# Kernel optimization log

Hardware: AMD Instinct MI355X
Metric: run time of the kernel (lower is better)

The kernel has to match this reference:

```python
import jax, jax.numpy as jnp
import numpy as np

MAX_DEPTH = 8          # inner-node depths 1..8; leaves at depth 9
LMBDA = 0.1            # args.lmbda; per-node lmbda = LMBDA * 2**(-depth)
EPS = 1e-6


def setup_inputs() -> dict:
    key = jax.random.key(0)
    ks = jax.random.split(key, 7)
    B, D, O = 16384, 2048, 1000
    n_inner = 2 ** MAX_DEPTH - 1   # 255
    n_leaf = 2 ** MAX_DEPTH       # 256
    x = jax.random.normal(ks[0], (B, D), dtype=jnp.float32)
    target = jax.random.randint(ks[1], (B,), 0, O)
    y = jax.nn.one_hot(target, O, dtype=jnp.float32)  # target_onehot
    W = jax.random.normal(ks[2], (n_inner, D), dtype=jnp.float32) / np.sqrt(D)
    b = jax.random.normal(ks[3], (n_inner,), dtype=jnp.float32) * 0.01
    beta = jax.random.normal(ks[4], (n_inner,), dtype=jnp.float32)
    leaf_params = jax.random.normal(ks[5], (n_leaf, O), dtype=jnp.float32)
    return {"x": x, "y": y, "W": W, "b": b, "beta": beta, "leaf_params": leaf_params}


def reference(x, y, W, b, beta, leaf_params):
    """Faithful vectorized version of SoftDecisionTree.cal_loss.
    Inner nodes are stored in level-order (heap) layout, left-to-right
    within each level, matching the left-first recursion of cal_prob.
    Returns (loss, output) like cal_loss.
    """
    B = x.shape[0]
    dt = x.dtype
    # All inner-node gates in one fused GEMM: sigmoid(beta * (x @ w + b))
    probs = jax.nn.sigmoid(beta * (x @ W.T + b))  # [B, n_inner]

    path = jnp.ones((B, 1), dt)  # path_prob_init
    C = jnp.asarray(0.0, dt)
    idx = 0
    for d in range(1, MAX_DEPTH + 1):  # small fixed loop over tree levels
        n = 2 ** (d - 1)
        p = probs[:, idx:idx + n]      # gate probs for this level's nodes [B, n]
        if d < MAX_DEPTH:              # get_penalty skips nodes whose children are leaves
            denom = jnp.sum(path, axis=0)                  # [n]
            denom = jnp.where(denom == 0, EPS, denom)
            alpha = jnp.sum(p * path, axis=0) / denom      # [n]
            alpha = jnp.clip(alpha, EPS, 1.0 - EPS)
            lmbda = LMBDA * 2.0 ** (-d)
            C = C - jnp.sum(lmbda * 0.5 * (jnp.log(alpha) + jnp.log1p(-alpha)))
        # children: left gets path*(1-p), right gets path*p, interleaved
        path = jnp.stack([path * (1.0 - p), path * p], axis=-1).reshape(B, 2 * n)
        idx += n
    # path: [B, n_leaf] leaf arrival probabilities (left-to-right leaf order)

    logQ = jax.nn.log_softmax(leaf_params, axis=-1)  # [n_leaf, O]
    TQ = y @ logQ.T                                  # [B, n_leaf]: y . log Q per leaf
    loss_term = jnp.mean(jnp.sum(path * TQ, axis=1))
    loss = -loss_term + C

    best = jnp.argmax(path, axis=1)   # first max, matches the '<' update order
    output = jnp.exp(logQ)[best]      # [B, O] max_Q
    return loss, output
```

## Files before the change

kernel.cpp:

```cpp
#include <hip/hip_runtime.h>


typedef __attribute__((ext_vector_type(8))) short short8;
typedef __attribute__((ext_vector_type(4))) float f32x4;

#define DIM 2048
#define NCLS 1000
#define NINNER 255
#define NPAD 256
#define BM 32
#define CHUNKF 128
#define NCHUNK 16

__device__ __forceinline__ unsigned cvt2bf(float a, float b) {
  return ((__float_as_uint(a) + 0x8000u) >> 16) | ((__float_as_uint(b) + 0x8000u) & 0xFFFF0000u);
}

__device__ __forceinline__ void async_copy16(const float* gsrc, void* ldst) {
  __builtin_amdgcn_global_load_lds(
      (const __attribute__((address_space(1))) unsigned int*)(gsrc),
      (__attribute__((address_space(3))) unsigned int*)(ldst), 16, 0, 0);
}

__global__ __launch_bounds__(256) void prep_w(const float* __restrict__ W,
                                              const float* __restrict__ b,
                                              const float* __restrict__ beta,
                                              unsigned short* __restrict__ WbP,
                                              float* __restrict__ bp,
                                              float* __restrict__ betap) {
  int f = blockIdx.x * 256 + threadIdx.x;
  int kt = f >> 10;
  int T = (f >> 6) & 15;
  int l = f & 63;
  int row = T * 16 + (l & 15);
  int k0 = kt * 32 + (l >> 4) * 8;
  uint4 o = make_uint4(0u, 0u, 0u, 0u);
  if (row < NINNER) {
    const float* src = W + (size_t)row * DIM + k0;
    o.x = cvt2bf(src[0], src[1]);
    o.y = cvt2bf(src[2], src[3]);
    o.z = cvt2bf(src[4], src[5]);
    o.w = cvt2bf(src[6], src[7]);
  }
  *(uint4*)(WbP + (size_t)f * 8) = o;
  if (f < NPAD) {
    bp[f] = (f < NINNER) ? b[f] : 0.f;
    betap[f] = (f < NINNER) ? beta[f] : 0.f;
  }
}

__global__ __launch_bounds__(256) void leaf_softmax(const float* __restrict__ leaf,
                                                    float* __restrict__ logQT,
                                                    float* __restrict__ Q) {
  int l = blockIdx.x, t = threadIdx.x;
  const float* row = leaf + (size_t)l * NCLS;
  __shared__ float red[256];
  float mx = -3.4e38f;
  for (int j = t; j < NCLS; j += 256) mx = fmaxf(mx, row[j]);
  red[t] = mx; __syncthreads();
  for (int s = 128; s; s >>= 1) { if (t < s) red[t] = fmaxf(red[t], red[t + s]); __syncthreads(); }
  mx = red[0]; __syncthreads();
  float sm = 0.f;
  for (int j = t; j < NCLS; j += 256) sm += __expf(row[j] - mx);
  red[t] = sm; __syncthreads();
  for (int s = 128; s; s >>= 1) { if (t < s) red[t] += red[t + s]; __syncthreads(); }
  float lse = mx + __logf(red[0]);
  for (int j = t; j < NCLS; j += 256) {
    float lg = row[j] - lse;
    logQT[(size_t)j * NPAD + l] = lg;
    Q[(size_t)l * NCLS + j] = __expf(lg);
  }
}

__global__ __launch_bounds__(256) void find_targets(const float* __restrict__ y,
                                                    int* __restrict__ tgt) {
  int wv = threadIdx.x >> 6, lane = threadIdx.x & 63;
  int r = blockIdx.x * 4 + wv;
  const float4* yr = (const float4*)(y + (size_t)r * NCLS);
  int found = 0x7fffffff;
#pragma unroll
  for (int i = 0; i < 4; ++i) {
    int j4 = i * 64 + lane;
    if (j4 < 250) {
      float4 v = yr[j4];
      if (v.x > 0.5f) found = min(found, 4 * j4 + 0);
      if (v.y > 0.5f) found = min(found, 4 * j4 + 1);
      if (v.z > 0.5f) found = min(found, 4 * j4 + 2);
      if (v.w > 0.5f) found = min(found, 4 * j4 + 3);
    }
  }
  for (int off = 32; off; off >>= 1) found = min(found, __shfl_down(found, off));
  if (lane == 0) tgt[r] = found;
}

__device__ __forceinline__ void chunk_mma(f32x4 (&ac)[2][4], const float* Ab,
                                          const unsigned short* bptr, int c,
                                          int frow, int fq) {
#pragma unroll
  for (int s = 0; s < 4; ++s) {
    int kt = c * 4 + s;
    short8 bfr[4];
#pragma unroll
    for (int nt = 0; nt < 4; ++nt)
      bfr[nt] = *(const short8*)(bptr + ((size_t)kt * 1024 + nt * 64) * 8);
    short8 afr[2];
#pragma unroll
    for (int mt = 0; mt < 2; ++mt) {
      int R = mt * 16 + frow;
      int r7 = R & 7;
      const float4* base = (const float4*)(Ab + R * 128 + s * 32);
      float4 va = base[(2 * fq) ^ r7];
      float4 vb = base[(2 * fq + 1) ^ r7];
      union { uint4 u; short8 s8; } cv;
      cv.u.x = cvt2bf(va.x, va.y);
      cv.u.y = cvt2bf(va.z, va.w);
      cv.u.z = cvt2bf(vb.x, vb.y);
      cv.u.w = cvt2bf(vb.z, vb.w);
      afr[mt] = cv.s8;
    }
#pragma unroll
    for (int nt = 0; nt < 4; ++nt)
#pragma unroll
      for (int mt = 0; mt < 2; ++mt)
        ac[mt][nt] = __builtin_amdgcn_mfma_f32_16x16x32_bf16(afr[mt], bfr[nt], ac[mt][nt], 0, 0, 0);
  }
}

__global__ __launch_bounds__(256, 2) void gemm_tree(
    const float* __restrict__ x, const unsigned short* __restrict__ WbP,
    const float* __restrict__ bp, const float* __restrict__ betap,
    const float* __restrict__ logQT, const int* __restrict__ tgt,
    float* __restrict__ acc, int* __restrict__ best) {
  __shared__ __align__(16) float As[2][4096];
  __shared__ float s0s[127], s1s[127], sdot;

  int tid = threadIdx.x;
  int lane = tid & 63, wave = tid >> 6;
  int frow = lane & 15, fq = lane >> 4;
  int m_base = blockIdx.x * BM;

  if (tid < 127) { s0s[tid] = 0.f; s1s[tid] = 0.f; }
  if (tid == 255) sdot = 0.f;

  const float* asrc[4];
  int aoff[4];
#pragma unroll
  for (int a = 0; a < 4; ++a) {
    int L = a * 4096 + tid * 16;
    int r = L >> 9;
    int j = (L >> 4) & 31;
    int c16 = (j & 24) | ((j & 7) ^ (r & 7));
    asrc[a] = x + (size_t)(m_base + r) * DIM + c16 * 4;
    aoff[a] = L;
  }

  const unsigned short* bptr = WbP + ((size_t)wave * 256 + lane) * 8;

  f32x4 accA[2][4] = {}, accB[2][4] = {};

#pragma unroll
  for (int a = 0; a < 4; ++a) async_copy16(asrc[a], (char*)As[0] + aoff[a]);
  __syncthreads();

  for (int c = 0; c < NCHUNK; ++c) {
    if (c + 1 < NCHUNK) {
      float* nb = As[(c + 1) & 1];
#pragma unroll
      for (int a = 0; a < 4; ++a)
        async_copy16(asrc[a] + (c + 1) * CHUNKF, (char*)nb + aoff[a]);
    }
    const float* Ab = As[c & 1];
    if (c < 8) chunk_mma(accA, Ab, bptr, c, frow, fq);
    else       chunk_mma(accB, Ab, bptr, c, frow, fq);
    __syncthreads();
  }

  float* Ps = &As[0][0];
#pragma unroll
  for (int mt = 0; mt < 2; ++mt)
#pragma unroll
    for (int nt = 0; nt < 4; ++nt)
#pragma unroll
      for (int rg = 0; rg < 4; ++rg)
        Ps[(mt * 16 + fq * 4 + rg) * 256 + wave * 64 + nt * 16 + frow] =
            accA[mt][nt][rg] + accB[mt][nt][rg];
  __syncthreads();

  {
    float bc = bp[tid], bec = betap[tid];
#pragma unroll 4
    for (int i = 0; i < 32; ++i) {
      float v = Ps[i * 256 + tid];
      Ps[i * 256 + tid] = 1.f / (1.f + __expf(-bec * (v + bc)));
    }
  }
  __syncthreads();

  float wdot = 0.f;
  float s0r[7] = {}, s1r[7] = {};
  for (int it = 0; it < 8; ++it) {
    int rl = wave * 8 + it;
    int r = m_base + rl;
    const float* wsp = Ps + rl * 256;
    int tg = tgt[r];
    float pp = 1.f;
#pragma unroll
    for (int d = 1; d <= 6; ++d) {
      int idx = (1 << (d - 1)) - 1 + (lane >> (7 - d));
      float p = wsp[idx];
      s0r[d - 1] += pp;
      s1r[d - 1] += p * pp;
      pp *= ((lane >> (6 - d)) & 1) ? p : (1.f - p);
    }
    float p7 = wsp[63 + lane];
    s0r[6] += pp;
    s1r[6] += p7 * pp;
    float pL = pp * (1.f - p7), pR = pp * p7;
    float p8a = wsp[127 + 2 * lane], p8b = wsp[128 + 2 * lane];
    float lf0 = pL * (1.f - p8a), lf1 = pL * p8a;
    float lf2 = pR * (1.f - p8b), lf3 = pR * p8b;
    float4 lq = *(const float4*)(logQT + (size_t)tg * NPAD + lane * 4);
    wdot += lf0 * lq.x + lf1 * lq.y + lf2 * lq.z + lf3 * lq.w;
    float bv = lf0; int bi = 4 * lane;
    if (lf1 > bv) { bv = lf1; bi = 4 * lane + 1; }
    if (lf2 > bv) { bv = lf2; bi = 4 * lane + 2; }
    if (lf3 > bv) { bv = lf3; bi = 4 * lane + 3; }
    for (int off = 32; off; off >>= 1) {
      float ov = __shfl_down(bv, off);
      int oi = __shfl_down(bi, off);
      if (ov > bv || (ov == bv && oi < bi)) { bv = ov; bi = oi; }
    }
    if (lane == 0) best[r] = bi;
  }
#pragma unroll
  for (int d = 1; d <= 6; ++d) {
    int idx = (1 << (d - 1)) - 1 + (lane >> (7 - d));
    if ((lane & ((1 << (7 - d)) - 1)) == 0) {
      atomicAdd(&s0s[idx], s0r[d - 1]);
      atomicAdd(&s1s[idx], s1r[d - 1]);
    }
  }
  atomicAdd(&s0s[63 + lane], s0r[6]);
  atomicAdd(&s1s[63 + lane], s1r[6]);
  for (int off = 32; off; off >>= 1) wdot += __shfl_down(wdot, off);
  if (lane == 0) atomicAdd(&sdot, wdot);
  __syncthreads();
  if (tid < 127) {
    atomicAdd(&acc[tid], s0s[tid]);
    atomicAdd(&acc[127 + tid], s1s[tid]);
  }
  if (tid == 255) atomicAdd(&acc[254], sdot);
}

__global__ __launch_bounds__(128) void finalize_loss(const float* __restrict__ acc,
                                                     float* __restrict__ out) {
  __shared__ float red[128];
  int t = threadIdx.x;
  float c = 0.f;
  if (t < 127) {
    float denom = acc[t];
    if (denom == 0.f) denom = 1e-6f;
    float alpha = acc[127 + t] / denom;
    alpha = fminf(fmaxf(alpha, 1e-6f), 1.f - 1e-6f);
    int d = 31 - __clz(t + 1) + 1;
    float lm = 0.1f * exp2f(-(float)d);
    c = -lm * 0.5f * (logf(alpha) + log1pf(-alpha));
  }
  red[t] = c;
  __syncthreads();
  for (int s = 64; s; s >>= 1) { if (t < s) red[t] += red[t + s]; __syncthreads(); }
  if (t == 0) out[0] = -(acc[254] / 16384.f) + red[0];
}

__global__ __launch_bounds__(256) void gather_rows(const float* __restrict__ Q,
                                                   const int* __restrict__ best,
                                                   float* __restrict__ out) {
  int wv = threadIdx.x >> 6, lane = threadIdx.x & 63;
  int r = blockIdx.x * 4 + wv;
  const float* src = Q + (size_t)best[r] * NCLS;
  float* dst = out + 1 + (size_t)r * NCLS;
  if (lane < 3) dst[lane] = src[lane];
  if (lane == 0) dst[999] = src[999];
#pragma unroll
  for (int i = 0; i < 4; ++i) {
    int q = i * 64 + lane;
    if (q < 249) {
      int o = 3 + 4 * q;
      float4 v = make_float4(src[o], src[o + 1], src[o + 2], src[o + 3]);
      *(float4*)(dst + o) = v;
    }
  }
}

extern "C" void kernel_launch(void* const* d_in, const int* in_sizes, int n_in,
                              void* d_out, int out_size, void* d_ws, size_t ws_size,
                              hipStream_t stream) {
  const float* x = (const float*)d_in[0];
  const float* y = (const float*)d_in[1];
  const float* W = (const float*)d_in[2];
  const float* b = (const float*)d_in[3];
  const float* beta = (const float*)d_in[4];
  const float* leaf = (const float*)d_in[5];
  float* out = (float*)d_out;
  char* ws = (char*)d_ws;

  unsigned short* WbP = (unsigned short*)(ws + 0);
  float* bp    = (float*)(ws + 1048576);
  float* betap = (float*)(ws + 1049600);
  float* accb  = (float*)(ws + 1050624);
  int* tgt     = (int*)(ws + 1051648);
  int* best    = (int*)(ws + 1117184);
  float* logQT = (float*)(ws + 1182720);
  float* Q     = (float*)(ws + 2206720);

  prep_w<<<256, 256, 0, stream>>>(W, b, beta, WbP, bp, betap);
  leaf_softmax<<<256, 256, 0, stream>>>(leaf, logQT, Q);
  find_targets<<<4096, 256, 0, stream>>>(y, tgt);
  hipMemsetAsync(accb, 0, 256 * sizeof(float), stream);
  gemm_tree<<<512, 256, 0, stream>>>(x, WbP, bp, betap, logQT, tgt, accb, best);
  finalize_loss<<<1, 128, 0, stream>>>(accb, out);
  gather_rows<<<4096, 256, 0, stream>>>(Q, best, out);
}
```

Baseline: 320.2 us.

## Triple-buffer x tiles with explicit vmcnt waits and prefetched W fragments

Moves the GEMM main loop from a double buffer to a triple-buffered LDS pipeline, so two chunks of x are in flight ahead of compute. Each chunk first issues all 16 W-fragment global loads, then the next async x copy, then waits with a partial s_waitcnt vmcnt and a raw s_barrier instead of a full __syncthreads. This is meant to hide global latency for both A and B operands behind the MFMA work. In exchange it uses more LDS (48KB), which may cut occupancy, and relies on hand-counted vmcnt values being right.

```diff
diff --git a/kernel.cpp b/kernel.cpp
--- a/kernel.cpp
+++ b/kernel.cpp
@@ -93,16 +93,26 @@
   if (lane == 0) tgt[r] = found;
 }
 
-__device__ __forceinline__ void chunk_mma(f32x4 (&ac)[2][4], const float* Ab,
-                                          const unsigned short* bptr, int c,
-                                          int frow, int fq) {
+template <int VW, bool PF>
+__device__ __forceinline__ void do_chunk(f32x4 (&ac)[2][4], const float* Ab,
+                                         const unsigned short* bc,
+                                         const float* const* ps, const int* aoff,
+                                         float* nbuf, int frow, int fq) {
+  short8 bfr[4][4];
+#pragma unroll
+  for (int s = 0; s < 4; ++s)
+#pragma unroll
+    for (int nt = 0; nt < 4; ++nt)
+      bfr[s][nt] = *(const short8*)(bc + s * 8192 + nt * 512);
+  asm volatile("" ::: "memory");
+  if (PF) {
+#pragma unroll
+    for (int a = 0; a < 4; ++a) async_copy16(ps[a], (char*)nbuf + aoff[a]);
+  }
+  asm volatile("s_waitcnt vmcnt(%0)" ::"n"(VW) : "memory");
+  __builtin_amdgcn_s_barrier();
 #pragma unroll
   for (int s = 0; s < 4; ++s) {
-    int kt = c * 4 + s;
-    short8 bfr[4];
-#pragma unroll
-    for (int nt = 0; nt < 4; ++nt)
-      bfr[nt] = *(const short8*)(bptr + ((size_t)kt * 1024 + nt * 64) * 8);
     short8 afr[2];
 #pragma unroll
     for (int mt = 0; mt < 2; ++mt) {
@@ -122,8 +132,10 @@
     for (int nt = 0; nt < 4; ++nt)
 #pragma unroll
       for (int mt = 0; mt < 2; ++mt)
-        ac[mt][nt] = __builtin_amdgcn_mfma_f32_16x16x32_bf16(afr[mt], bfr[nt], ac[mt][nt], 0, 0, 0);
-  }
+        ac[mt][nt] = __builtin_amdgcn_mfma_f32_16x16x32_bf16(afr[mt], bfr[s][nt], ac[mt][nt], 0, 0, 0);
+  }
+  __builtin_amdgcn_sched_barrier(0);
+  __builtin_amdgcn_s_barrier();
 }
 
 __global__ __launch_bounds__(256, 2) void gemm_tree(
@@ -131,7 +143,7 @@
     const float* __restrict__ bp, const float* __restrict__ betap,
     const float* __restrict__ logQT, const int* __restrict__ tgt,
     float* __restrict__ acc, int* __restrict__ best) {
-  __shared__ __align__(16) float As[2][4096];
+  __shared__ __align__(16) float As[3][4096];
   __shared__ float s0s[127], s1s[127], sdot;
 
   int tid = threadIdx.x;
@@ -160,20 +172,35 @@
 
 #pragma unroll
   for (int a = 0; a < 4; ++a) async_copy16(asrc[a], (char*)As[0] + aoff[a]);
-  __syncthreads();
-
-  for (int c = 0; c < NCHUNK; ++c) {
-    if (c + 1 < NCHUNK) {
-      float* nb = As[(c + 1) & 1];
-#pragma unroll
-      for (int a = 0; a < 4; ++a)
-        async_copy16(asrc[a] + (c + 1) * CHUNKF, (char*)nb + aoff[a]);
-    }
-    const float* Ab = As[c & 1];
-    if (c < 8) chunk_mma(accA, Ab, bptr, c, frow, fq);
-    else       chunk_mma(accB, Ab, bptr, c, frow, fq);
-    __syncthreads();
-  }
+#pragma unroll
+  for (int a = 0; a < 4; ++a) async_copy16(asrc[a] + CHUNKF, (char*)As[1] + aoff[a]);
+
+  float *bA = As[0], *bB = As[1], *bC = As[2];
+  const float* ps[4];
+#pragma unroll
+  for (int a = 0; a < 4; ++a) ps[a] = asrc[a] + 2 * CHUNKF;
+  const unsigned short* bc = bptr;
+
+  for (int c = 0; c < 8; ++c) {
+    do_chunk<24, true>(accA, bA, bc, ps, aoff, bC, frow, fq);
+    float* t = bA; bA = bB; bB = bC; bC = t;
+    bc += 32768;
+#pragma unroll
+    for (int a = 0; a < 4; ++a) ps[a] += CHUNKF;
+  }
+  for (int c = 0; c < 6; ++c) {
+    do_chunk<24, true>(accB, bA, bc, ps, aoff, bC, frow, fq);
+    float* t = bA; bA = bB; bB = bC; bC = t;
+    bc += 32768;
+#pragma unroll
+    for (int a = 0; a < 4; ++a) ps[a] += CHUNKF;
+  }
+  do_chunk<20, false>(accB, bA, bc, ps, aoff, bC, frow, fq);
+  { float* t = bA; bA = bB; bB = bC; bC = t; }
+  bc += 32768;
+  do_chunk<16, false>(accB, bA, bc, ps, aoff, bC, frow, fq);
+
+  __syncthreads();
 
   float* Ps = &As[0][0];
 #pragma unroll
@@ -187,11 +214,11 @@
   __syncthreads();
 
   {
-    float bc = bp[tid], bec = betap[tid];
+    float bc2 = bp[tid], bec = betap[tid];
 #pragma unroll 4
     for (int i = 0; i < 32; ++i) {
       float v = Ps[i * 256 + tid];
-      Ps[i * 256 + tid] = 1.f / (1.f + __expf(-bec * (v + bc)));
+      Ps[i * 256 + tid] = 1.f / (1.f + __expf(-bec * (v + bc2)));
     }
   }
   __syncthreads();
```

New measurement: 311.7 us. 2.6% less time.

## Load A fragments directly from global into registers with software pipelining, dropping LDS staging

Applied to the files above, without the earlier changes.

The x tile is now loaded straight from global memory into registers for each MFMA fragment, with a four-stage register pipeline (three k-steps of lookahead), instead of async-copying it into double-buffered shared memory with a barrier per chunk. This removes the LDS round trip and the per-chunk __syncthreads, and shrinks shared memory to the probability buffer. In exchange every wave reads x independently, so all four waves fetch the same A rows and rely on cache for reuse. It also raises register pressure, which could hurt the two-blocks-per-CU occupancy target.

```diff
diff --git a/kernel.cpp b/kernel.cpp
--- a/kernel.cpp
+++ b/kernel.cpp
@@ -9,17 +9,9 @@
 #define NINNER 255
 #define NPAD 256
 #define BM 32
-#define CHUNKF 128
-#define NCHUNK 16
 
 __device__ __forceinline__ unsigned cvt2bf(float a, float b) {
   return ((__float_as_uint(a) + 0x8000u) >> 16) | ((__float_as_uint(b) + 0x8000u) & 0xFFFF0000u);
-}
-
-__device__ __forceinline__ void async_copy16(const float* gsrc, void* ldst) {
-  __builtin_amdgcn_global_load_lds(
-      (const __attribute__((address_space(1))) unsigned int*)(gsrc),
-      (__attribute__((address_space(3))) unsigned int*)(ldst), 16, 0, 0);
 }
 
 __global__ __launch_bounds__(256) void prep_w(const float* __restrict__ W,
@@ -93,45 +85,44 @@
   if (lane == 0) tgt[r] = found;
 }
 
-__device__ __forceinline__ void chunk_mma(f32x4 (&ac)[2][4], const float* Ab,
-                                          const unsigned short* bptr, int c,
-                                          int frow, int fq) {
-#pragma unroll
-  for (int s = 0; s < 4; ++s) {
-    int kt = c * 4 + s;
-    short8 bfr[4];
-#pragma unroll
-    for (int nt = 0; nt < 4; ++nt)
-      bfr[nt] = *(const short8*)(bptr + ((size_t)kt * 1024 + nt * 64) * 8);
-    short8 afr[2];
-#pragma unroll
-    for (int mt = 0; mt < 2; ++mt) {
-      int R = mt * 16 + frow;
-      int r7 = R & 7;
-      const float4* base = (const float4*)(Ab + R * 128 + s * 32);
-      float4 va = base[(2 * fq) ^ r7];
-      float4 vb = base[(2 * fq + 1) ^ r7];
-      union { uint4 u; short8 s8; } cv;
-      cv.u.x = cvt2bf(va.x, va.y);
-      cv.u.y = cvt2bf(va.z, va.w);
-      cv.u.z = cvt2bf(vb.x, vb.y);
-      cv.u.w = cvt2bf(vb.z, vb.w);
-      afr[mt] = cv.s8;
-    }
-#pragma unroll
-    for (int nt = 0; nt < 4; ++nt)
-#pragma unroll
-      for (int mt = 0; mt < 2; ++mt)
-        ac[mt][nt] = __builtin_amdgcn_mfma_f32_16x16x32_bf16(afr[mt], bfr[nt], ac[mt][nt], 0, 0, 0);
-  }
-}
+#define DECLF(S) float4 S##a00, S##a01, S##a10, S##a11; short8 S##b0, S##b1, S##b2, S##b3;
+
+#define LOADK(S, kt) do {                                                    \
+  const float* _a0 = arow0 + (size_t)(kt) * 32;                              \
+  const float* _a1 = arow1 + (size_t)(kt) * 32;                              \
+  S##a00 = *(const float4*)_a0;  S##a01 = *(const float4*)(_a0 + 4);         \
+  S##a10 = *(const float4*)_a1;  S##a11 = *(const float4*)(_a1 + 4);         \
+  const unsigned short* _b = bptr + (size_t)(kt) * 8192;                     \
+  S##b0 = *(const short8*)(_b);        S##b1 = *(const short8*)(_b + 512);   \
+  S##b2 = *(const short8*)(_b + 1024); S##b3 = *(const short8*)(_b + 1536);  \
+} while (0)
+
+#define COMPUTE(S, AC) do {                                                  \
+  short8 _afr0, _afr1;                                                       \
+  { union { uint4 u; short8 s; } cv;                                         \
+    cv.u.x = cvt2bf(S##a00.x, S##a00.y); cv.u.y = cvt2bf(S##a00.z, S##a00.w);\
+    cv.u.z = cvt2bf(S##a01.x, S##a01.y); cv.u.w = cvt2bf(S##a01.z, S##a01.w);\
+    _afr0 = cv.s; }                                                          \
+  { union { uint4 u; short8 s; } cv;                                         \
+    cv.u.x = cvt2bf(S##a10.x, S##a10.y); cv.u.y = cvt2bf(S##a10.z, S##a10.w);\
+    cv.u.z = cvt2bf(S##a11.x, S##a11.y); cv.u.w = cvt2bf(S##a11.z, S##a11.w);\
+    _afr1 = cv.s; }                                                          \
+  AC[0][0] = __builtin_amdgcn_mfma_f32_16x16x32_bf16(_afr0, S##b0, AC[0][0], 0, 0, 0); \
+  AC[1][0] = __builtin_amdgcn_mfma_f32_16x16x32_bf16(_afr1, S##b0, AC[1][0], 0, 0, 0); \
+  AC[0][1] = __builtin_amdgcn_mfma_f32_16x16x32_bf16(_afr0, S##b1, AC[0][1], 0, 0, 0); \
+  AC[1][1] = __builtin_amdgcn_mfma_f32_16x16x32_bf16(_afr1, S##b1, AC[1][1], 0, 0, 0); \
+  AC[0][2] = __builtin_amdgcn_mfma_f32_16x16x32_bf16(_afr0, S##b2, AC[0][2], 0, 0, 0); \
+  AC[1][2] = __builtin_amdgcn_mfma_f32_16x16x32_bf16(_afr1, S##b2, AC[1][2], 0, 0, 0); \
+  AC[0][3] = __builtin_amdgcn_mfma_f32_16x16x32_bf16(_afr0, S##b3, AC[0][3], 0, 0, 0); \
+  AC[1][3] = __builtin_amdgcn_mfma_f32_16x16x32_bf16(_afr1, S##b3, AC[1][3], 0, 0, 0); \
+} while (0)
 
 __global__ __launch_bounds__(256, 2) void gemm_tree(
     const float* __restrict__ x, const unsigned short* __restrict__ WbP,
     const float* __restrict__ bp, const float* __restrict__ betap,
     const float* __restrict__ logQT, const int* __restrict__ tgt,
     float* __restrict__ acc, int* __restrict__ best) {
-  __shared__ __align__(16) float As[2][4096];
+  __shared__ __align__(16) float Ps[32 * 256];
   __shared__ float s0s[127], s1s[127], sdot;
 
   int tid = threadIdx.x;
@@ -142,40 +133,32 @@
   if (tid < 127) { s0s[tid] = 0.f; s1s[tid] = 0.f; }
   if (tid == 255) sdot = 0.f;
 
-  const float* asrc[4];
-  int aoff[4];
-#pragma unroll
-  for (int a = 0; a < 4; ++a) {
-    int L = a * 4096 + tid * 16;
-    int r = L >> 9;
-    int j = (L >> 4) & 31;
-    int c16 = (j & 24) | ((j & 7) ^ (r & 7));
-    asrc[a] = x + (size_t)(m_base + r) * DIM + c16 * 4;
-    aoff[a] = L;
-  }
-
+  const float* arow0 = x + (size_t)(m_base + frow) * DIM + fq * 8;
+  const float* arow1 = arow0 + (size_t)16 * DIM;
   const unsigned short* bptr = WbP + ((size_t)wave * 256 + lane) * 8;
 
   f32x4 accA[2][4] = {}, accB[2][4] = {};
 
-#pragma unroll
-  for (int a = 0; a < 4; ++a) async_copy16(asrc[a], (char*)As[0] + aoff[a]);
-  __syncthreads();
-
-  for (int c = 0; c < NCHUNK; ++c) {
-    if (c + 1 < NCHUNK) {
-      float* nb = As[(c + 1) & 1];
-#pragma unroll
-      for (int a = 0; a < 4; ++a)
-        async_copy16(asrc[a] + (c + 1) * CHUNKF, (char*)nb + aoff[a]);
-    }
-    const float* Ab = As[c & 1];
-    if (c < 8) chunk_mma(accA, Ab, bptr, c, frow, fq);
-    else       chunk_mma(accB, Ab, bptr, c, frow, fq);
-    __syncthreads();
-  }
-
-  float* Ps = &As[0][0];
+  DECLF(s0_) DECLF(s1_) DECLF(s2_) DECLF(s3_)
+  LOADK(s0_, 0); LOADK(s1_, 1); LOADK(s2_, 2);
+
+  for (int kt = 0; kt < 32; kt += 4) {
+    LOADK(s3_, kt + 3);
+    COMPUTE(s0_, accA); LOADK(s0_, kt + 4);
+    COMPUTE(s1_, accA); LOADK(s1_, kt + 5);
+    COMPUTE(s2_, accA); LOADK(s2_, kt + 6);
+    COMPUTE(s3_, accA);
+  }
+  for (int kt = 32; kt < 64; kt += 4) {
+    LOADK(s3_, kt + 3);
+    COMPUTE(s0_, accB); if (kt < 60) LOADK(s0_, kt + 4);
+    COMPUTE(s1_, accB); if (kt < 60) LOADK(s1_, kt + 5);
+    COMPUTE(s2_, accB); if (kt < 60) LOADK(s2_, kt + 6);
+    COMPUTE(s3_, accB);
+  }
+
+  __syncthreads();
+
 #pragma unroll
   for (int mt = 0; mt < 2; ++mt)
 #pragma unroll
@@ -187,11 +170,11 @@
   __syncthreads();
 
   {
-    float bc = bp[tid], bec = betap[tid];
+    float bc2 = bp[tid], bec = betap[tid];
 #pragma unroll 4
     for (int i = 0; i < 32; ++i) {
       float v = Ps[i * 256 + tid];
-      Ps[i * 256 + tid] = 1.f / (1.f + __expf(-bec * (v + bc)));
+      Ps[i * 256 + tid] = 1.f / (1.f + __expf(-bec * (v + bc2)));
     }
   }
   __syncthreads();
```

Result: slower. 339.8 us (+6.1%).
